# Performance work log

Hardware: AMD Instinct MI355X
Metric: run time of the kernel (lower is better)

The kernel has to match this reference:

```python
import jax, jax.numpy as jnp
import numpy as np
import math

D_EMBED = 1024
N_HEADS = 16
HEAD_DIM = D_EMBED // N_HEADS
ROPE_BASE = 10000.0


def apply_rope(x):
    # x: [B, S, H, D] ; torchtune-style interleaved RoPE
    B, S, H, D = x.shape
    half = D // 2
    inv_freq = 1.0 / (ROPE_BASE ** (jnp.arange(0, D, 2, dtype=jnp.float32) / D))  # [half]
    angles = jnp.arange(S, dtype=jnp.float32)[:, None] * inv_freq[None, :]        # [S, half]
    cos = jnp.cos(angles)[None, :, None, :].astype(x.dtype)  # [1,S,1,half]
    sin = jnp.sin(angles)[None, :, None, :].astype(x.dtype)
    x1 = x[..., 0::2]
    x2 = x[..., 1::2]
    o1 = x1 * cos - x2 * sin
    o2 = x1 * sin + x2 * cos
    return jnp.stack([o1, o2], axis=-1).reshape(B, S, H, D)


def setup_inputs() -> dict:
    key = jax.random.key(0)
    ks = jax.random.split(key, 7)
    B, S = 4, 2048
    d_tri = D_EMBED
    q = jax.random.normal(ks[0], (B, S, 2 * d_tri), dtype=jnp.float32)
    k = jax.random.normal(ks[1], (B, S, 2 * d_tri), dtype=jnp.float32)
    v = jax.random.normal(ks[2], (B, S, d_tri), dtype=jnp.float32)
    s_in = 1.0 / math.sqrt(2 * d_tri)
    s_tri = 1.0 / math.sqrt(d_tri)
    W_q = jax.random.normal(ks[3], (D_EMBED, 2 * d_tri), dtype=jnp.float32) * s_in
    W_k = jax.random.normal(ks[4], (D_EMBED, 2 * d_tri), dtype=jnp.float32) * s_in
    W_v = jax.random.normal(ks[5], (d_tri, d_tri), dtype=jnp.float32) * s_tri
    W_o = jax.random.normal(ks[6], (d_tri, d_tri), dtype=jnp.float32) * s_tri
    return {"q": q, "k": k, "v": v, "W_q": W_q, "W_k": W_k, "W_v": W_v, "W_o": W_o}


def reference(q, k, v, W_q, W_k, W_v, W_o):
    B, S, _ = q.shape
    H, Dh = N_HEADS, HEAD_DIM
    scale = 1.0 / math.sqrt(D_EMBED)

    qp = (q @ W_q.T).reshape(B, S, H, Dh)
    kp = (k @ W_k.T).reshape(B, S, H, Dh)
    vp = (v @ W_v.T).reshape(B, S, H, Dh)

    qp = apply_rope(qp)
    kp = apply_rope(kp)

    # [B,H,S,S]
    scores = jnp.einsum('bqhd,bkhd->bhqk', qp, kp) * scale
    causal = jnp.tril(jnp.ones((S, S), dtype=bool))
    scores = jnp.where(causal[None, None], scores, -jnp.inf)
    probs = jax.nn.softmax(scores, axis=-1)
    # dropout layers are identity in eval mode
    out = jnp.einsum('bhqk,bkhd->bqhd', probs, vp).reshape(B, S, D_EMBED)
    return out @ W_o.T
```

## Files before the change

kernel.cpp:

```cpp
#include <hip/hip_runtime.h>
#include <math.h>

#define S_LEN 2048
#define DEMB  1024
#define DH    64

typedef short bf16x8 __attribute__((ext_vector_type(8)));
typedef short bf16x4 __attribute__((ext_vector_type(4)));
typedef float floatx4 __attribute__((ext_vector_type(4)));

__device__ __forceinline__ short f2bf(float f) {
    unsigned u = __builtin_bit_cast(unsigned, f);
    u += 0x7FFFu + ((u >> 16) & 1u);
    return (short)(u >> 16);
}

__global__ void rope_table_k(float2* __restrict__ tab) {
    int idx = blockIdx.x * 256 + threadIdx.x;
    int s = idx >> 5, i = idx & 31;
    double ang = (double)s * pow(10000.0, -(double)i / 32.0);
    tab[idx] = make_float2((float)cos(ang), (float)sin(ang));
}

struct CvtArgs { const float* src[7]; short* dst[7]; int n[7]; };
__global__ __launch_bounds__(256) void cvt_k(CvtArgs a) {
    int seg = blockIdx.y;
    int idx = (blockIdx.x * 256 + threadIdx.x) * 8;
    if (idx >= a.n[seg]) return;
    const float4* s = (const float4*)(a.src[seg] + idx);
    float4 v0 = s[0], v1 = s[1];
    bf16x8 r;
    r[0] = f2bf(v0.x); r[1] = f2bf(v0.y); r[2] = f2bf(v0.z); r[3] = f2bf(v0.w);
    r[4] = f2bf(v1.x); r[5] = f2bf(v1.y); r[6] = f2bf(v1.z); r[7] = f2bf(v1.w);
    *(bf16x8*)(a.dst[seg] + idx) = r;
}

__device__ __forceinline__ void gld16(const void* g, void* l) {
    __builtin_amdgcn_global_load_lds(
        (const __attribute__((address_space(1))) void*)g,
        (__attribute__((address_space(3))) void*)l, 16, 0, 0);
}

template<int EPI>
__device__ __forceinline__ void gemm_body(
    const short* __restrict__ A, const short* __restrict__ B,
    void* __restrict__ Cout, const float2* __restrict__ rope_tab,
    int K, short* smem)
{
    short* sA = smem;
    short* sB = smem + 8192;

    const int tid  = threadIdx.x;
    const int lane = tid & 63;
    const int wv   = tid >> 6;
    const int wm   = wv >> 1, wn = wv & 1;
    const int lr   = lane & 15, quad = lane >> 4;
    const int m0   = blockIdx.y * 128, n0 = blockIdx.x * 128;
    const int N    = 1024;

    const short* gA[4]; const short* gB[4];
    #pragma unroll
    for (int j = 0; j < 4; j++) {
        int c = j * 256 + tid;
        int row = c >> 3, sp = c & 7;
        int cs = (sp ^ (row & 7)) * 8;
        gA[j] = A + (size_t)(m0 + row) * K + cs;
        gB[j] = B + (size_t)(n0 + row) * K + cs;
    }

    floatx4 acc[4][4] = {};

    for (int k0 = 0; k0 < K; k0 += 64) {
        #pragma unroll
        for (int j = 0; j < 4; j++) {
            gld16(gA[j] + k0, sA + j * 2048 + wv * 512);
            gld16(gB[j] + k0, sB + j * 2048 + wv * 512);
        }
        __syncthreads();
        bf16x8 af[4][2], bfr[4][2];
        #pragma unroll
        for (int t = 0; t < 4; t++)
            #pragma unroll
            for (int ks = 0; ks < 2; ks++) {
                int ph = (ks * 4 + quad) ^ (lr & 7);
                af[t][ks]  = *reinterpret_cast<const bf16x8*>(&sA[(wm * 64 + t * 16 + lr) * 64 + ph * 8]);
                bfr[t][ks] = *reinterpret_cast<const bf16x8*>(&sB[(wn * 64 + t * 16 + lr) * 64 + ph * 8]);
            }
        #pragma unroll
        for (int ks = 0; ks < 2; ks++)
            #pragma unroll
            for (int mt = 0; mt < 4; mt++)
                #pragma unroll
                for (int nt = 0; nt < 4; nt++)
                    acc[mt][nt] = __builtin_amdgcn_mfma_f32_16x16x32_bf16(af[mt][ks], bfr[nt][ks], acc[mt][nt], 0, 0, 0);
        __syncthreads();
    }

    if constexpr (EPI == 0) {
        unsigned* sTi = (unsigned*)smem;
        #pragma unroll
        for (int nt = 0; nt < 4; nt++) {
            int n_l = wn * 64 + nt * 16 + lr;
            int ii  = ((n0 + n_l) & 63) >> 1;
            #pragma unroll
            for (int mt = 0; mt < 4; mt++)
                #pragma unroll
                for (int r = 0; r < 4; r++) {
                    int row_l = wm * 64 + mt * 16 + quad * 4 + r;
                    float2 cs = rope_tab[((m0 + row_l) & (S_LEN - 1)) * 32 + ii];
                    float v  = acc[mt][nt][r];
                    float vn = __shfl_xor(v, 1);
                    float o0 = v * cs.x - vn * cs.y;
                    float o1 = vn * cs.x + v * cs.y;
                    if (!(lr & 1)) {
                        unsigned pk = (unsigned)(unsigned short)f2bf(o0) |
                                      ((unsigned)(unsigned short)f2bf(o1) << 16);
                        sTi[row_l * 68 + (n_l >> 1)] = pk;
                    }
                }
        }
        __syncthreads();
        short* C = (short*)Cout;
        #pragma unroll
        for (int j = 0; j < 8; j++) {
            int c = j * 256 + tid;
            int row = c >> 4, col = (c & 15) * 8;
            bf16x8 val = *reinterpret_cast<const bf16x8*>(&smem[row * 136 + col]);
            *reinterpret_cast<bf16x8*>(&C[(size_t)(m0 + row) * N + n0 + col]) = val;
        }
    } else if constexpr (EPI == 2) {
        float* C = (float*)Cout;
        #pragma unroll
        for (int mt = 0; mt < 4; mt++)
            #pragma unroll
            for (int r = 0; r < 4; r++) {
                size_t rowoff = (size_t)(m0 + wm * 64 + mt * 16 + quad * 4 + r) * N;
                #pragma unroll
                for (int nt = 0; nt < 4; nt++)
                    C[rowoff + n0 + wn * 64 + nt * 16 + lr] = acc[mt][nt][r];
            }
    } else {
        short* sT = smem;
        #pragma unroll
        for (int nt = 0; nt < 4; nt++) {
            int nl = wn * 64 + nt * 16 + lr;
            #pragma unroll
            for (int mt = 0; mt < 4; mt++)
                #pragma unroll
                for (int r = 0; r < 4; r++)
                    sT[nl * 136 + wm * 64 + mt * 16 + quad * 4 + r] = f2bf(acc[mt][nt][r]);
        }
        __syncthreads();
        short* C = (short*)Cout;
        int bb = m0 >> 11;
        int s_base = m0 & (S_LEN - 1);
        #pragma unroll
        for (int i = 0; i < 8; i++) {
            int col = (tid >> 4) + i * 16;
            int mc  = (tid & 15) * 8;
            bf16x8 v = *reinterpret_cast<const bf16x8*>(&sT[col * 136 + mc]);
            size_t row = (size_t)bb * DEMB + (n0 + col);
            *reinterpret_cast<bf16x8*>(&C[row * S_LEN + s_base + mc]) = v;
        }
    }
}

__global__ __launch_bounds__(256, 3) void gemm_proj(
    const short* __restrict__ Aq, const short* __restrict__ Bq, void* __restrict__ Cq,
    const short* __restrict__ Ak, const short* __restrict__ Bk, void* __restrict__ Ck,
    const short* __restrict__ Av, const short* __restrict__ Bv, void* __restrict__ Cv,
    const float2* __restrict__ rope_tab)
{
    __shared__ __align__(16) short smem[17408];
    if (blockIdx.z == 0)
        gemm_body<0>(Aq, Bq, Cq, rope_tab, 2048, smem);
    else if (blockIdx.z == 1)
        gemm_body<0>(Ak, Bk, Ck, rope_tab, 2048, smem);
    else
        gemm_body<1>(Av, Bv, Cv, nullptr, 1024, smem);
}

__global__ __launch_bounds__(256, 3) void gemm_out(
    const short* __restrict__ A, const short* __restrict__ B, void* __restrict__ Cout)
{
    __shared__ __align__(16) short smem[17408];
    gemm_body<2>(A, B, Cout, nullptr, 1024, smem);
}

__global__ __launch_bounds__(256, 2) void flash_k(
    const short* __restrict__ qp, const short* __restrict__ kp,
    const short* __restrict__ vpT, short* __restrict__ attn)
{
    __shared__ __align__(16) short sPb[4][2048];

    const int tid = threadIdx.x;
    const int w = tid >> 6, lane = tid & 63, lr = lane & 15, quad = lane >> 4;
    const int g = blockIdx.x;
    const int bh = (g & 7) | ((g >> 7) << 3);
    const int tq = (g >> 3) & 15;
    const int qt = (tq < 8) ? (15 - tq) : (tq - 8);
    const int b = bh >> 4, h = bh & 15;
    const int R = qt * 128 + w * 32;
    const size_t qbase = (size_t)(b * S_LEN) * DEMB + h * DH;

    const short* kbase = kp + qbase;
    const short* vbase = vpT + ((size_t)(b * DEMB) + h * DH) * S_LEN;

    bf16x8 qf[2][2];
    #pragma unroll
    for (int mt = 0; mt < 2; mt++)
        #pragma unroll
        for (int ks = 0; ks < 2; ks++)
            qf[mt][ks] = *reinterpret_cast<const bf16x8*>(
                &qp[qbase + (size_t)(R + mt * 16 + lr) * DEMB + ks * 32 + quad * 8]);

    floatx4 oacc[2][4] = {};
    float lsum[2][4] = {};
    const float CEXP = 0.045084220081510574f;
    short* pw = sPb[w];

    const int myend = (R + 31) >> 6;

    for (int kt = 0; kt <= myend; kt++) {
        const short* kT = kbase + (size_t)kt * 64 * DEMB;
        const short* vT = vbase + kt * 64;

        floatx4 st[2][4];
        __builtin_amdgcn_s_setprio(1);
        #pragma unroll
        for (int nt = 0; nt < 4; nt++) {
            const short* kr = kT + (size_t)(nt * 16 + lr) * DEMB + quad * 8;
            bf16x8 kf0 = *reinterpret_cast<const bf16x8*>(kr);
            bf16x8 kf1 = *reinterpret_cast<const bf16x8*>(kr + 32);
            #pragma unroll
            for (int mt = 0; mt < 2; mt++) {
                floatx4 z = {};
                z = __builtin_amdgcn_mfma_f32_16x16x32_bf16(qf[mt][0], kf0, z, 0, 0, 0);
                st[mt][nt] = __builtin_amdgcn_mfma_f32_16x16x32_bf16(qf[mt][1], kf1, z, 0, 0, 0);
            }
        }
        __builtin_amdgcn_s_setprio(0);

        const bool need_mask = (kt * 64 + 63 > R);
        #pragma unroll
        for (int mt = 0; mt < 2; mt++)
            #pragma unroll
            for (int nt = 0; nt < 4; nt++)
                #pragma unroll
                for (int r = 0; r < 4; r++) {
                    float t = fminf(st[mt][nt][r] * CEXP, 80.f);
                    float p = __builtin_amdgcn_exp2f(t);
                    if (need_mask) {
                        int col = kt * 64 + nt * 16 + lr;
                        int row = R + mt * 16 + quad * 4 + r;
                        p = (col > row) ? 0.f : p;
                    }
                    st[mt][nt][r] = p;
                    lsum[mt][r] += p;
                }

        bf16x8 vf[4][2];
        #pragma unroll
        for (int d = 0; d < 4; d++) {
            const short* vr = vT + (size_t)(d * 16 + lr) * S_LEN + quad * 8;
            vf[d][0] = *reinterpret_cast<const bf16x8*>(vr);
            vf[d][1] = *reinterpret_cast<const bf16x8*>(vr + 32);
        }

        #pragma unroll
        for (int mt = 0; mt < 2; mt++)
            #pragma unroll
            for (int nt = 0; nt < 4; nt++)
                #pragma unroll
                for (int r = 0; r < 4; r++) {
                    int rw = mt * 16 + quad * 4 + r;
                    int chunk = (nt * 2 + (lr >> 3)) ^ (rw & 7);
                    pw[rw * 64 + chunk * 8 + (lr & 7)] = f2bf(st[mt][nt][r]);
                }

        bf16x8 pf[2][2];
        #pragma unroll
        for (int mt = 0; mt < 2; mt++)
            #pragma unroll
            for (int ks = 0; ks < 2; ks++) {
                int rr = mt * 16 + lr;
                int c  = (ks * 4 + quad) ^ (rr & 7);
                pf[mt][ks] = *reinterpret_cast<const bf16x8*>(&pw[rr * 64 + c * 8]);
            }

        __builtin_amdgcn_s_setprio(1);
        #pragma unroll
        for (int d = 0; d < 4; d++)
            #pragma unroll
            for (int mt = 0; mt < 2; mt++) {
                oacc[mt][d] = __builtin_amdgcn_mfma_f32_16x16x32_bf16(pf[mt][0], vf[d][0], oacc[mt][d], 0, 0, 0);
                oacc[mt][d] = __builtin_amdgcn_mfma_f32_16x16x32_bf16(pf[mt][1], vf[d][1], oacc[mt][d], 0, 0, 0);
            }
        __builtin_amdgcn_s_setprio(0);
    }

    #pragma unroll
    for (int mt = 0; mt < 2; mt++)
        #pragma unroll
        for (int r = 0; r < 4; r++) {
            float l = lsum[mt][r];
            l += __shfl_xor(l, 1);
            l += __shfl_xor(l, 2);
            l += __shfl_xor(l, 4);
            l += __shfl_xor(l, 8);
            float inv = 1.f / l;
            size_t rowoff = qbase + (size_t)(R + mt * 16 + quad * 4 + r) * DEMB;
            #pragma unroll
            for (int d = 0; d < 4; d++)
                attn[rowoff + d * 16 + lr] = f2bf(oacc[mt][d][r] * inv);
        }
}

__device__ __forceinline__ bf16x4 load4(const float* p) {
    const float4 v = *reinterpret_cast<const float4*>(p);
    bf16x4 r; r[0] = f2bf(v.x); r[1] = f2bf(v.y); r[2] = f2bf(v.z); r[3] = f2bf(v.w);
    return r;
}
__device__ __forceinline__ bf16x4 load4(const short* p) {
    return *reinterpret_cast<const bf16x4*>(p);
}

template<typename TA, int EPI>
__global__ __launch_bounds__(256) void gemm_nt(
    const TA* __restrict__ A, const float* __restrict__ B,
    void* __restrict__ Cout, const float2* __restrict__ rope_tab,
    int M, int N, int K)
{
    __shared__ __align__(16) short smem[(EPI == 1) ? (128 * 136) : (2 * 128 * 40)];
    short* sA = smem;
    short* sB = smem + 128 * 40;

    const int tid  = threadIdx.x;
    const int lane = tid & 63;
    const int wv   = tid >> 6;
    const int wm   = wv >> 1, wn = wv & 1;
    const int lr   = lane & 15, quad = lane >> 4;
    const int m0   = blockIdx.y * 128, n0 = blockIdx.x * 128;

    floatx4 acc[4][4] = {};

    for (int k0 = 0; k0 < K; k0 += 32) {
        #pragma unroll
        for (int i = 0; i < 4; i++) {
            int c = tid + i * 256;
            int row = c >> 3, kc = (c & 7) << 2;
            bf16x4 v = load4(&A[(size_t)(m0 + row) * K + k0 + kc]);
            *reinterpret_cast<bf16x4*>(&sA[row * 40 + kc]) = v;
        }
        #pragma unroll
        for (int i = 0; i < 4; i++) {
            int c = tid + i * 256;
            int row = c >> 3, kc = (c & 7) << 2;
            bf16x4 v = load4(&B[(size_t)(n0 + row) * K + k0 + kc]);
            *reinterpret_cast<bf16x4*>(&sB[row * 40 + kc]) = v;
        }
        __syncthreads();
        bf16x8 af[4], bfr[4];
        #pragma unroll
        for (int t = 0; t < 4; t++)
            af[t] = *reinterpret_cast<const bf16x8*>(&sA[(wm * 64 + t * 16 + lr) * 40 + quad * 8]);
        #pragma unroll
        for (int t = 0; t < 4; t++)
            bfr[t] = *reinterpret_cast<const bf16x8*>(&sB[(wn * 64 + t * 16 + lr) * 40 + quad * 8]);
        #pragma unroll
        for (int mt = 0; mt < 4; mt++)
            #pragma unroll
            for (int nt = 0; nt < 4; nt++)
                acc[mt][nt] = __builtin_amdgcn_mfma_f32_16x16x32_bf16(af[mt], bfr[nt], acc[mt][nt], 0, 0, 0);
        __syncthreads();
    }

    if constexpr (EPI == 0) {
        short* C = (short*)Cout;
        #pragma unroll
        for (int nt = 0; nt < 4; nt++) {
            int n_g = n0 + wn * 64 + nt * 16 + lr;
            int ii  = (n_g & 63) >> 1;
            bool evenc = (n_g & 1) == 0;
            #pragma unroll
            for (int mt = 0; mt < 4; mt++) {
                #pragma unroll
                for (int r = 0; r < 4; r++) {
                    int m_g = m0 + wm * 64 + mt * 16 + quad * 4 + r;
                    float2 cs = rope_tab[(m_g & (S_LEN - 1)) * 32 + ii];
                    float v  = acc[mt][nt][r];
                    float vn = __shfl_xor(v, 1);
                    float o = evenc ? (v * cs.x - vn * cs.y) : (v * cs.x + vn * cs.y);
                    C[(size_t)m_g * N + n_g] = f2bf(o);
                }
            }
        }
    } else if constexpr (EPI == 2) {
        float* C = (float*)Cout;
        #pragma unroll
        for (int mt = 0; mt < 4; mt++)
            #pragma unroll
            for (int r = 0; r < 4; r++) {
                size_t rowoff = (size_t)(m0 + wm * 64 + mt * 16 + quad * 4 + r) * N;
                #pragma unroll
                for (int nt = 0; nt < 4; nt++)
                    C[rowoff + n0 + wn * 64 + nt * 16 + lr] = acc[mt][nt][r];
            }
    } else {
        short* sT = smem;
        __syncthreads();
        #pragma unroll
        for (int nt = 0; nt < 4; nt++) {
            int nl = wn * 64 + nt * 16 + lr;
            #pragma unroll
            for (int mt = 0; mt < 4; mt++)
                #pragma unroll
                for (int r = 0; r < 4; r++)
                    sT[nl * 136 + wm * 64 + mt * 16 + quad * 4 + r] = f2bf(acc[mt][nt][r]);
        }
        __syncthreads();
        short* C = (short*)Cout;
        int bb = m0 >> 11;
        int s_base = m0 & (S_LEN - 1);
        #pragma unroll
        for (int i = 0; i < 8; i++) {
            int col = (tid >> 4) + i * 16;
            int mc  = (tid & 15) * 8;
            bf16x8 v = *reinterpret_cast<const bf16x8*>(&sT[col * 136 + mc]);
            size_t row = (size_t)bb * DEMB + (n0 + col);
            *reinterpret_cast<bf16x8*>(&C[row * S_LEN + s_base + mc]) = v;
        }
    }
}

extern "C" void kernel_launch(void* const* d_in, const int* in_sizes, int n_in,
                              void* d_out, int out_size, void* d_ws, size_t ws_size,
                              hipStream_t stream) {
    const float* q  = (const float*)d_in[0];
    const float* k  = (const float*)d_in[1];
    const float* v  = (const float*)d_in[2];
    const float* Wq = (const float*)d_in[3];
    const float* Wk = (const float*)d_in[4];
    const float* Wv = (const float*)d_in[5];
    const float* Wo = (const float*)d_in[6];
    float* out = (float*)d_out;

    char* ws = (char*)d_ws;
    const size_t MB = 1024 * 1024;
    short*  qp   = (short*)(ws);
    short*  kp   = (short*)(ws + 16 * MB);
    short*  vpT  = (short*)(ws + 32 * MB);
    short*  attn = (short*)(ws + 48 * MB);
    float2* tab  = (float2*)(ws + 64 * MB);

    rope_table_k<<<256, 256, 0, stream>>>(tab);

    dim3 g2(8, 64);
    if (ws_size >= 157 * MB) {
        short* qb  = (short*)(ws + 65 * MB);
        short* kb  = (short*)(ws + 97 * MB);
        short* vb  = (short*)(ws + 129 * MB);
        short* wqb = (short*)(ws + 145 * MB);
        short* wkb = (short*)(ws + 149 * MB);
        short* wvb = (short*)(ws + 153 * MB);
        short* wob = (short*)(ws + 155 * MB);

        CvtArgs ca;
        ca.src[0] = q;  ca.dst[0] = qb;  ca.n[0] = 16777216;
        ca.src[1] = k;  ca.dst[1] = kb;  ca.n[1] = 16777216;
        ca.src[2] = v;  ca.dst[2] = vb;  ca.n[2] = 8388608;
        ca.src[3] = Wq; ca.dst[3] = wqb; ca.n[3] = 2097152;
        ca.src[4] = Wk; ca.dst[4] = wkb; ca.n[4] = 2097152;
        ca.src[5] = Wv; ca.dst[5] = wvb; ca.n[5] = 1048576;
        ca.src[6] = Wo; ca.dst[6] = wob; ca.n[6] = 1048576;
        cvt_k<<<dim3(8192, 7), 256, 0, stream>>>(ca);

        gemm_proj<<<dim3(8, 64, 3), 256, 0, stream>>>(
            qb, wqb, qp, kb, wkb, kp, vb, wvb, vpT, tab);
        flash_k<<<1024, 256, 0, stream>>>(qp, kp, vpT, attn);
        gemm_out<<<g2, 256, 0, stream>>>(attn, wob, out);
    } else {
        gemm_nt<float, 0><<<g2, 256, 0, stream>>>(q, Wq, qp,  tab,     8192, 1024, 2048);
        gemm_nt<float, 0><<<g2, 256, 0, stream>>>(k, Wk, kp,  tab,     8192, 1024, 2048);
        gemm_nt<float, 1><<<g2, 256, 0, stream>>>(v, Wv, vpT, nullptr, 8192, 1024, 1024);
        flash_k<<<1024, 256, 0, stream>>>(qp, kp, vpT, attn);
        gemm_nt<short, 2><<<g2, 256, 0, stream>>>(attn, Wo, out, nullptr, 8192, 1024, 1024);
    }
}
```

Baseline: 524.1 us.

## Prefetch next K tile in attention loop and remap GEMM blocks per XCD

The attention inner loop now loads the K fragments for the following tile into registers right after the QK MFMAs, so that global-load latency overlaps with the softmax and PV work instead of stalling the start of each iteration. Separately, the GEMM block index is remapped so that consecutive M row-blocks land on the same XCD, which is meant to improve L2 reuse of A tiles. The prefetch adds 8 bf16x8 registers per lane and may lower occupancy. The remapping assumes an 8x64 block grid.

```diff
diff --git a/kernel.cpp b/kernel.cpp
--- a/kernel.cpp
+++ b/kernel.cpp
@@ -55,7 +55,10 @@
     const int wv   = tid >> 6;
     const int wm   = wv >> 1, wn = wv & 1;
     const int lr   = lane & 15, quad = lane >> 4;
-    const int m0   = blockIdx.y * 128, n0 = blockIdx.x * 128;
+    const int bid = blockIdx.x + (blockIdx.y << 3);
+    const int xcd = bid & 7, loc = bid >> 3;
+    const int m0  = (xcd * 8 + (loc >> 3)) * 128;
+    const int n0  = (loc & 7) * 128;
     const int N    = 1024;
 
     const short* gA[4]; const short* gB[4];
@@ -221,25 +224,40 @@
 
     const int myend = (R + 31) >> 6;
 
+    bf16x8 kf[4][2];
+    #pragma unroll
+    for (int nt = 0; nt < 4; nt++) {
+        const short* kr = kbase + (size_t)(nt * 16 + lr) * DEMB + quad * 8;
+        kf[nt][0] = *reinterpret_cast<const bf16x8*>(kr);
+        kf[nt][1] = *reinterpret_cast<const bf16x8*>(kr + 32);
+    }
+
     for (int kt = 0; kt <= myend; kt++) {
-        const short* kT = kbase + (size_t)kt * 64 * DEMB;
         const short* vT = vbase + kt * 64;
 
         floatx4 st[2][4];
         __builtin_amdgcn_s_setprio(1);
         #pragma unroll
-        for (int nt = 0; nt < 4; nt++) {
-            const short* kr = kT + (size_t)(nt * 16 + lr) * DEMB + quad * 8;
-            bf16x8 kf0 = *reinterpret_cast<const bf16x8*>(kr);
-            bf16x8 kf1 = *reinterpret_cast<const bf16x8*>(kr + 32);
+        for (int nt = 0; nt < 4; nt++)
             #pragma unroll
             for (int mt = 0; mt < 2; mt++) {
                 floatx4 z = {};
-                z = __builtin_amdgcn_mfma_f32_16x16x32_bf16(qf[mt][0], kf0, z, 0, 0, 0);
-                st[mt][nt] = __builtin_amdgcn_mfma_f32_16x16x32_bf16(qf[mt][1], kf1, z, 0, 0, 0);
-            }
-        }
+                z = __builtin_amdgcn_mfma_f32_16x16x32_bf16(qf[mt][0], kf[nt][0], z, 0, 0, 0);
+                st[mt][nt] = __builtin_amdgcn_mfma_f32_16x16x32_bf16(qf[mt][1], kf[nt][1], z, 0, 0, 0);
+            }
         __builtin_amdgcn_s_setprio(0);
+
+        bf16x8 kn[4][2];
+        {
+            const int ktn = (kt < myend) ? (kt + 1) : myend;
+            const short* kTn = kbase + (size_t)ktn * 64 * DEMB;
+            #pragma unroll
+            for (int nt = 0; nt < 4; nt++) {
+                const short* kr = kTn + (size_t)(nt * 16 + lr) * DEMB + quad * 8;
+                kn[nt][0] = *reinterpret_cast<const bf16x8*>(kr);
+                kn[nt][1] = *reinterpret_cast<const bf16x8*>(kr + 32);
+            }
+        }
 
         const bool need_mask = (kt * 64 + 63 > R);
         #pragma unroll
@@ -297,6 +315,12 @@
                 oacc[mt][d] = __builtin_amdgcn_mfma_f32_16x16x32_bf16(pf[mt][1], vf[d][1], oacc[mt][d], 0, 0, 0);
             }
         __builtin_amdgcn_s_setprio(0);
+
+        #pragma unroll
+        for (int nt = 0; nt < 4; nt++) {
+            kf[nt][0] = kn[nt][0];
+            kf[nt][1] = kn[nt][1];
+        }
     }
 
     #pragma unroll
```

Result: no change. 517.7 us (-1.2%).

## Store K and V projections in MFMA-fragment tiled layout and remap GEMM blocks per XCD

Applied to the files above, without the earlier changes.

The K and V projection epilogues now write their outputs in a pre-swizzled per-(batch, head, 64-token tile) layout that matches the MFMA operand fragments. The flash kernel can then load each K/V fragment as one contiguous 16-byte chunk per lane instead of doing strided row reads. The GEMM block indexing is also remapped so that consecutive blocks on the same XCD share A rows, to improve L2 reuse. The cost is more index arithmetic in the epilogues and scattered 16-byte stores during projection.

```diff
diff --git a/kernel.cpp b/kernel.cpp
--- a/kernel.cpp
+++ b/kernel.cpp
@@ -55,7 +55,10 @@
     const int wv   = tid >> 6;
     const int wm   = wv >> 1, wn = wv & 1;
     const int lr   = lane & 15, quad = lane >> 4;
-    const int m0   = blockIdx.y * 128, n0 = blockIdx.x * 128;
+    const int bid = blockIdx.x + (blockIdx.y << 3);
+    const int xcd = bid & 7, loc = bid >> 3;
+    const int m0  = (xcd * 8 + (loc >> 3)) * 128;
+    const int n0  = (loc & 7) * 128;
     const int N    = 1024;
 
     const short* gA[4]; const short* gB[4];
@@ -96,7 +99,7 @@
         __syncthreads();
     }
 
-    if constexpr (EPI == 0) {
+    if constexpr (EPI == 0 || EPI == 3) {
         unsigned* sTi = (unsigned*)smem;
         #pragma unroll
         for (int nt = 0; nt < 4; nt++) {
@@ -124,9 +127,22 @@
         #pragma unroll
         for (int j = 0; j < 8; j++) {
             int c = j * 256 + tid;
-            int row = c >> 4, col = (c & 15) * 8;
-            bf16x8 val = *reinterpret_cast<const bf16x8*>(&smem[row * 136 + col]);
-            *reinterpret_cast<bf16x8*>(&C[(size_t)(m0 + row) * N + n0 + col]) = val;
+            int row = c >> 4, col8 = (c & 15) * 8;
+            bf16x8 val = *reinterpret_cast<const bf16x8*>(&smem[row * 136 + col8]);
+            if constexpr (EPI == 0) {
+                *reinterpret_cast<bf16x8*>(&C[(size_t)(m0 + row) * N + n0 + col8]) = val;
+            } else {
+                int tok = m0 + row;
+                int bb  = tok >> 11;
+                int s   = tok & (S_LEN - 1);
+                int ktt = s >> 6, tokr = s & 63;
+                int ff  = n0 + col8;
+                int hh  = ff >> 6, fr = ff & 63;
+                int nt_ = tokr >> 4, lr_ = tokr & 15;
+                int ks_ = fr >> 5,  qd_ = (fr & 31) >> 3;
+                size_t base = ((size_t)((bb * 16 + hh) * 32 + ktt)) << 12;
+                *reinterpret_cast<bf16x8*>(&C[base + ((nt_ * 2 + ks_) << 9) + (qd_ * 16 + lr_) * 8]) = val;
+            }
         }
     } else if constexpr (EPI == 2) {
         float* C = (float*)Cout;
@@ -159,8 +175,13 @@
             int col = (tid >> 4) + i * 16;
             int mc  = (tid & 15) * 8;
             bf16x8 v = *reinterpret_cast<const bf16x8*>(&sT[col * 136 + mc]);
-            size_t row = (size_t)bb * DEMB + (n0 + col);
-            *reinterpret_cast<bf16x8*>(&C[row * S_LEN + s_base + mc]) = v;
+            int s   = s_base + mc;
+            int ktt = s >> 6, tokr = s & 63;
+            int ff  = n0 + col, hh = ff >> 6, fr = ff & 63;
+            int d_  = fr >> 4, lr_ = fr & 15;
+            int ks_ = tokr >> 5, qd_ = (tokr & 31) >> 3;
+            size_t base = ((size_t)((bb * 16 + hh) * 32 + ktt)) << 12;
+            *reinterpret_cast<bf16x8*>(&C[base + ((d_ * 2 + ks_) << 9) + (qd_ * 16 + lr_) * 8]) = v;
         }
     }
 }
@@ -175,7 +196,7 @@
     if (blockIdx.z == 0)
         gemm_body<0>(Aq, Bq, Cq, rope_tab, 2048, smem);
     else if (blockIdx.z == 1)
-        gemm_body<0>(Ak, Bk, Ck, rope_tab, 2048, smem);
+        gemm_body<3>(Ak, Bk, Ck, rope_tab, 2048, smem);
     else
         gemm_body<1>(Av, Bv, Cv, nullptr, 1024, smem);
 }
@@ -203,8 +224,9 @@
     const int R = qt * 128 + w * 32;
     const size_t qbase = (size_t)(b * S_LEN) * DEMB + h * DH;
 
-    const short* kbase = kp + qbase;
-    const short* vbase = vpT + ((size_t)(b * DEMB) + h * DH) * S_LEN;
+    const short* kblk = kp  + (((size_t)(b * 16 + h)) << 17);
+    const short* vblk = vpT + (((size_t)(b * 16 + h)) << 17);
+    const int l8 = lane * 8;
 
     bf16x8 qf[2][2];
     #pragma unroll
@@ -222,16 +244,15 @@
     const int myend = (R + 31) >> 6;
 
     for (int kt = 0; kt <= myend; kt++) {
-        const short* kT = kbase + (size_t)kt * 64 * DEMB;
-        const short* vT = vbase + kt * 64;
+        const short* kT = kblk + ((size_t)kt << 12);
+        const short* vT = vblk + ((size_t)kt << 12);
 
         floatx4 st[2][4];
         __builtin_amdgcn_s_setprio(1);
         #pragma unroll
         for (int nt = 0; nt < 4; nt++) {
-            const short* kr = kT + (size_t)(nt * 16 + lr) * DEMB + quad * 8;
-            bf16x8 kf0 = *reinterpret_cast<const bf16x8*>(kr);
-            bf16x8 kf1 = *reinterpret_cast<const bf16x8*>(kr + 32);
+            bf16x8 kf0 = *reinterpret_cast<const bf16x8*>(kT + ((nt * 2 + 0) << 9) + l8);
+            bf16x8 kf1 = *reinterpret_cast<const bf16x8*>(kT + ((nt * 2 + 1) << 9) + l8);
             #pragma unroll
             for (int mt = 0; mt < 2; mt++) {
                 floatx4 z = {};
@@ -248,8 +269,8 @@
             for (int nt = 0; nt < 4; nt++)
                 #pragma unroll
                 for (int r = 0; r < 4; r++) {
-                    float t = fminf(st[mt][nt][r] * CEXP, 80.f);
-                    float p = __builtin_amdgcn_exp2f(t);
+                    float tv = fminf(st[mt][nt][r] * CEXP, 80.f);
+                    float p = __builtin_amdgcn_exp2f(tv);
                     if (need_mask) {
                         int col = kt * 64 + nt * 16 + lr;
                         int row = R + mt * 16 + quad * 4 + r;
@@ -262,9 +283,8 @@
         bf16x8 vf[4][2];
         #pragma unroll
         for (int d = 0; d < 4; d++) {
-            const short* vr = vT + (size_t)(d * 16 + lr) * S_LEN + quad * 8;
-            vf[d][0] = *reinterpret_cast<const bf16x8*>(vr);
-            vf[d][1] = *reinterpret_cast<const bf16x8*>(vr + 32);
+            vf[d][0] = *reinterpret_cast<const bf16x8*>(vT + ((d * 2 + 0) << 9) + l8);
+            vf[d][1] = *reinterpret_cast<const bf16x8*>(vT + ((d * 2 + 1) << 9) + l8);
         }
 
         #pragma unroll
@@ -375,7 +395,7 @@
         __syncthreads();
     }
 
-    if constexpr (EPI == 0) {
+    if constexpr (EPI == 0 || EPI == 3) {
         short* C = (short*)Cout;
         #pragma unroll
         for (int nt = 0; nt < 4; nt++) {
@@ -391,7 +411,17 @@
                     float v  = acc[mt][nt][r];
                     float vn = __shfl_xor(v, 1);
                     float o = evenc ? (v * cs.x - vn * cs.y) : (v * cs.x + vn * cs.y);
-                    C[(size_t)m_g * N + n_g] = f2bf(o);
+                    if constexpr (EPI == 0) {
+                        C[(size_t)m_g * N + n_g] = f2bf(o);
+                    } else {
+                        int bb = m_g >> 11, s = m_g & (S_LEN - 1);
+                        int ktt = s >> 6, tokr = s & 63;
+                        int hh = n_g >> 6, fr = n_g & 63;
+                        int nt_ = tokr >> 4, lr_ = tokr & 15;
+                        int ks_ = fr >> 5, qd_ = (fr & 31) >> 3, j_ = fr & 7;
+                        size_t base = ((size_t)((bb * 16 + hh) * 32 + ktt)) << 12;
+                        C[base + ((nt_ * 2 + ks_) << 9) + (qd_ * 16 + lr_) * 8 + j_] = f2bf(o);
+                    }
                 }
             }
         }
@@ -427,8 +457,13 @@
             int col = (tid >> 4) + i * 16;
             int mc  = (tid & 15) * 8;
             bf16x8 v = *reinterpret_cast<const bf16x8*>(&sT[col * 136 + mc]);
-            size_t row = (size_t)bb * DEMB + (n0 + col);
-            *reinterpret_cast<bf16x8*>(&C[row * S_LEN + s_base + mc]) = v;
+            int s   = s_base + mc;
+            int ktt = s >> 6, tokr = s & 63;
+            int ff  = n0 + col, hh = ff >> 6, fr = ff & 63;
+            int d_  = fr >> 4, lr_ = fr & 15;
+            int ks_ = tokr >> 5, qd_ = (tokr & 31) >> 3;
+            size_t base = ((size_t)((bb * 16 + hh) * 32 + ktt)) << 12;
+            *reinterpret_cast<bf16x8*>(&C[base + ((d_ * 2 + ks_) << 9) + (qd_ * 16 + lr_) * 8]) = v;
         }
     }
 }
@@ -481,7 +516,7 @@
         gemm_out<<<g2, 256, 0, stream>>>(attn, wob, out);
     } else {
         gemm_nt<float, 0><<<g2, 256, 0, stream>>>(q, Wq, qp,  tab,     8192, 1024, 2048);
-        gemm_nt<float, 0><<<g2, 256, 0, stream>>>(k, Wk, kp,  tab,     8192, 1024, 2048);
+        gemm_nt<float, 3><<<g2, 256, 0, stream>>>(k, Wk, kp,  tab,     8192, 1024, 2048);
         gemm_nt<float, 1><<<g2, 256, 0, stream>>>(v, Wv, vpT, nullptr, 8192, 1024, 1024);
         flash_k<<<1024, 256, 0, stream>>>(qp, kp, vpT, attn);
         gemm_nt<short, 2><<<g2, 256, 0, stream>>>(attn, Wo, out, nullptr, 8192, 1024, 1024);
```

Result: faster. 427.2 us (-18.5%).
